# Kernel optimization log

Measured on AMD Instinct MI355X. Metric: run time of the kernel, lower is better.

Reference implementation:

```python
import jax, jax.numpy as jnp
import numpy as np

N_SLICES, H, W = 64, 64, 64
VD, VH, VW = 64, 64, 64
K = 3            # PSF kernel size per axis
RES = 1.5        # res_s / res_r
GAP = 1.0        # through-plane slice spacing in recon voxels
N_ITER = 2       # CG iterations (init kwarg)


def _rotmat(ax, ay, az):
    cx, sx = np.cos(ax), np.sin(ax)
    cy, sy = np.cos(ay), np.sin(ay)
    cz, sz = np.cos(az), np.sin(az)
    Rx = np.array([[1, 0, 0], [0, cx, -sx], [0, sx, cx]])
    Ry = np.array([[cy, 0, sy], [0, 1, 0], [-sy, 0, cy]])
    Rz = np.array([[cz, -sz, 0], [sz, cz, 0], [0, 0, 1]])
    return Rz @ Ry @ Rx


def setup_inputs() -> dict:
    rng = np.random.default_rng(0)
    R = np.stack([_rotmat(*rng.normal(0.0, 0.05, 3)) for _ in range(N_SLICES)])
    t = np.zeros((N_SLICES, 3))
    t[:, :2] = rng.normal(0.0, 1.0, (N_SLICES, 2))
    t[:, 2] = (np.arange(N_SLICES) - (N_SLICES - 1) / 2) * GAP + rng.normal(0.0, 0.3, N_SLICES)
    transforms = jnp.asarray(np.concatenate([R, t[:, :, None]], -1), jnp.float32)  # (S,3,4)
    k1, k2 = jax.random.split(jax.random.key(0))
    slices = jax.random.uniform(k1, (N_SLICES, H, W), jnp.float32)
    volume = jax.random.uniform(k2, (VD, VH, VW), jnp.float32) * 0.1
    g = np.arange(K) - (K - 1) / 2
    gz, gy, gx = np.meshgrid(g, g, g, indexing='ij')
    psf = np.exp(-(gx ** 2 + gy ** 2) / (2 * 0.6 ** 2) - gz ** 2 / (2 * 1.0 ** 2))
    psf = jnp.asarray(psf / psf.sum(), jnp.float32)
    return {"transforms": transforms, "slices": slices, "volume": volume, "psf": psf}


def _positions(transforms):
    # PSF sample positions of every slice pixel, mapped into volume voxel coords (xyz).
    xs = (jnp.arange(W) - (W - 1) / 2) * RES
    ys = (jnp.arange(H) - (H - 1) / 2) * RES
    o = jnp.arange(K) - (K - 1) / 2
    oz, oy, ox = jnp.meshgrid(o, o, o, indexing='ij')
    off = jnp.stack([ox, oy, oz], -1).reshape(-1, 3)              # (K^3, 3)
    base = jnp.stack(jnp.broadcast_arrays(xs[None, :], ys[:, None], jnp.zeros((H, W))), -1)
    pts = base[None] + off[:, None, None, :]                      # (K^3, H, W, 3) slice frame
    R, tr = transforms[:, :, :3], transforms[:, :, 3]
    pos = jnp.einsum('sij,khwj->skhwi', R, pts) + tr[:, None, None, None, :]
    center = jnp.array([(VW - 1) / 2, (VH - 1) / 2, (VD - 1) / 2], jnp.float32)
    return pos + center                                           # (S, K^3, H, W, 3)


def _corner_iter(pos):
    # yields the 8 trilinear corners: (clipped int indices (z,y,x), weight with OOB zeroed)
    x, y, z = pos[..., 0], pos[..., 1], pos[..., 2]
    x0, y0, z0 = jnp.floor(x), jnp.floor(y), jnp.floor(z)
    fx, fy, fz = x - x0, y - y0, z - z0
    for dz in (0, 1):
        for dy in (0, 1):
            for dx in (0, 1):
                xi, yi, zi = x0 + dx, y0 + dy, z0 + dz
                w = (fx if dx else 1 - fx) * (fy if dy else 1 - fy) * (fz if dz else 1 - fz)
                valid = (xi >= 0) & (xi < VW) & (yi >= 0) & (yi < VH) & (zi >= 0) & (zi < VD)
                w = jnp.where(valid, w, 0.0)
                yield (jnp.clip(zi, 0, VD - 1).astype(jnp.int32),
                       jnp.clip(yi, 0, VH - 1).astype(jnp.int32),
                       jnp.clip(xi, 0, VW - 1).astype(jnp.int32)), w


def _A(vol, pos, psf_flat):
    # slice_acquisition: trilinear gather + PSF-weighted sum -> (S,H,W)
    acc = jnp.zeros(pos.shape[:-1], vol.dtype)
    for (zi, yi, xi), w in _corner_iter(pos):
        acc = acc + w * vol[zi, yi, xi]
    return jnp.einsum('k,skhw->shw', psf_flat, acc)


def _At(slc, pos, psf_flat):
    # slice_acquisition_adjoint: PSF-weighted trilinear scatter-add -> (VD,VH,VW)
    vals = psf_flat[None, :, None, None] * slc[:, None]           # (S,K^3,H,W)
    vol = jnp.zeros((VD, VH, VW), slc.dtype)
    for (zi, yi, xi), w in _corner_iter(pos):
        vol = vol.at[zi, yi, xi].add(w * vals)
    return vol


def _cg(Afun, b, x0, n_iter):
    x = x0
    r = b - Afun(x)
    p = r
    rr = jnp.vdot(r, r)
    for i in range(n_iter):
        Ap = Afun(p)
        alpha = rr / jnp.vdot(p, Ap)
        x = x + alpha * p
        if i == n_iter - 1:
            break
        r = r - alpha * Ap
        rr_new = jnp.vdot(r, r)
        p = r + (rr_new / rr) * p
        rr = rr_new
    return x


def reference(transforms, slices, volume, psf):
    pos = _positions(transforms)
    psf_flat = psf.reshape(-1)
    AtA = lambda v: _At(_A(v, pos, psf_flat), pos, psf_flat)
    b = _At(slices, pos, psf_flat)
    x = _cg(AtA, b, volume, N_ITER)
    return jax.nn.relu(x)
```

## Files before the change

### kernel.cpp

```cpp
#include <hip/hip_runtime.h>

typedef __attribute__((ext_vector_type(2))) float f32x2;

#define NS 64
#define HH 64
#define WW 64
#define VD 64
#define VH 64
#define VW 64
#define NVOX (VD*VH*VW)
#define NPIX (NS*HH*WW)
#define RES 1.5f
#define NTAB (NS*27)
#define WIN 6
#define SPLIT 4
#define COL_PAD 67
#define GP_ROW 68
#define GP_SLC (66*GP_ROW)
#define GP_TOT (NS*GP_SLC)

__global__ __launch_bounds__(256) void k_setup(const float* __restrict__ tr,
                                               const float* __restrict__ psf,
                                               float* __restrict__ tab) {
    int i = blockIdx.x * 256 + threadIdx.x;
    if (i >= NTAB) return;
    int s = i / 27, k = i % 27;
    const float* p = tr + s * 12;
    float R00 = p[0], R01 = p[1], R02 = p[2],  t0 = p[3];
    float R10 = p[4], R11 = p[5], R12 = p[6],  t1 = p[7];
    float R20 = p[8], R21 = p[9], R22 = p[10], t2 = p[11];
    float Ux = RES * R00, Uy = RES * R10, Uz = RES * R20;
    float Vx = RES * R01, Vy = RES * R11, Vz = RES * R21;
    float ox = (float)(k % 3 - 1), oy = (float)((k / 3) % 3 - 1), oz = (float)(k / 9 - 1);
    float Cx = t0 + 31.5f + R00 * ox + R01 * oy + R02 * oz - 31.5f * (Ux + Vx);
    float Cy = t1 + 31.5f + R10 * ox + R11 * oy + R12 * oz - 31.5f * (Uy + Vy);
    float Cz = t2 + 31.5f + R20 * ox + R21 * oy + R22 * oz - 31.5f * (Uz + Vz);
    float inv = 1.f / (Ux * Vy - Uy * Vx);
    float* e = tab + i * 16;
    e[0] = Vy * inv;  e[1] = -Uy * inv;  e[2] = -Vx * inv; e[3] = Ux * inv;
    e[4] = Ux; e[5] = Uy; e[6] = Vx; e[7] = Vy;
    e[8] = Uz; e[9] = Vz; e[10] = Cx; e[11] = Cy;
    e[12] = Cz; e[13] = psf[k]; e[14] = 0.f; e[15] = 0.f;
}

__device__ __forceinline__ float trilin_gather_bf(const float* __restrict__ vol,
                                                  float px, float py, float pz) {
    float x0 = floorf(px), y0 = floorf(py), z0 = floorf(pz);
    float fx = px - x0, fy = py - y0, fz = pz - z0;
    int ix = (int)x0, iy = (int)y0, iz = (int)z0;

    float wx0 = ((unsigned)ix       < 64u) ? (1.f - fx) : 0.f;
    float wx1 = ((unsigned)(ix + 1) < 64u) ? fx         : 0.f;
    float wy0 = ((unsigned)iy       < 64u) ? (1.f - fy) : 0.f;
    float wy1 = ((unsigned)(iy + 1) < 64u) ? fy         : 0.f;
    float wz0 = ((unsigned)iz       < 64u) ? (1.f - fz) : 0.f;
    float wz1 = ((unsigned)(iz + 1) < 64u) ? fz         : 0.f;

    int xc0 = min(max(ix, 0), 63),     xc1 = min(max(ix + 1, 0), 63);
    int yc0 = min(max(iy, 0), 63) << 6,  yc1 = min(max(iy + 1, 0), 63) << 6;
    int zc0 = min(max(iz, 0), 63) << 12, zc1 = min(max(iz + 1, 0), 63) << 12;

    float v000 = vol[zc0 + yc0 + xc0], v001 = vol[zc0 + yc0 + xc1];
    float v010 = vol[zc0 + yc1 + xc0], v011 = vol[zc0 + yc1 + xc1];
    float v100 = vol[zc1 + yc0 + xc0], v101 = vol[zc1 + yc0 + xc1];
    float v110 = vol[zc1 + yc1 + xc0], v111 = vol[zc1 + yc1 + xc1];

    float w00 = wx0 * wy0, w01 = wx1 * wy0, w10 = wx0 * wy1, w11 = wx1 * wy1;
    float lo = fmaf(w00, v000, fmaf(w01, v001, fmaf(w10, v010, w11 * v011)));
    float hi = fmaf(w00, v100, fmaf(w01, v101, fmaf(w10, v110, w11 * v111)));
    return fmaf(wz0, lo, wz1 * hi);
}

template<bool SUB>
__global__ __launch_bounds__(256) void k_a(const float* __restrict__ vin,
                                           float* __restrict__ gp,
                                           const float* __restrict__ tr,
                                           const float* __restrict__ psf,
                                           const float* __restrict__ slc) {
    __shared__ float s_psf[27];
    if (threadIdx.x < 27) s_psf[threadIdx.x] = psf[threadIdx.x];
    __syncthreads();
    int gid = blockIdx.x * 256 + threadIdx.x;
    int pixel = gid >> 2, q = gid & 3;
    int s = pixel >> 12;
    int pix = pixel & 4095;
    int h = pix >> 6, w = pix & 63;
    const float* p = tr + s * 12;
    float R0 = p[0], R1 = p[1], R2 = p[2],  t0 = p[3];
    float R3 = p[4], R4 = p[5], R5 = p[6],  t1 = p[7];
    float R6 = p[8], R7 = p[9], R8 = p[10], t2 = p[11];
    float xs = ((float)w - 31.5f) * RES;
    float ys = ((float)h - 31.5f) * RES;
    float p0x = fmaf(R0, xs, fmaf(R1, ys, t0)) + 31.5f;
    float p0y = fmaf(R3, xs, fmaf(R4, ys, t1)) + 31.5f;
    float p0z = fmaf(R6, xs, fmaf(R7, ys, t2)) + 31.5f;
    float a = 0.f;
#pragma unroll
    for (int j = 0; j < 7; ++j) {
        int k = q + 4 * j;
        if (k < 27) {
            float ox = (float)(k % 3 - 1), oy = (float)((k / 3) % 3 - 1), oz = (float)(k / 9 - 1);
            float px = p0x + ox * R0 + oy * R1 + oz * R2;
            float py = p0y + ox * R3 + oy * R4 + oz * R5;
            float pz = p0z + ox * R6 + oy * R7 + oz * R8;
            a = fmaf(s_psf[k], trilin_gather_bf(vin, px, py, pz), a);
        }
    }
    a += __shfl_xor(a, 1);
    a += __shfl_xor(a, 2);
    if (q == 0) gp[s * GP_SLC + (h + 1) * GP_ROW + (w + 1)] = SUB ? (slc[pixel] - a) : a;
}

__device__ __forceinline__ void block_reduce_atomic(float v, float* dst) {
#pragma unroll
    for (int off = 32; off > 0; off >>= 1) v += __shfl_down(v, off, 64);
    __shared__ float s_red[4];
    int lane = threadIdx.x & 63, wid = threadIdx.x >> 6;
    if (lane == 0) s_red[wid] = v;
    __syncthreads();
    if (threadIdx.x == 0) atomicAdd(dst, s_red[0] + s_red[1] + s_red[2] + s_red[3]);
}

__global__ __launch_bounds__(512, 4) void k_atv(const float* __restrict__ g,
                                                float* __restrict__ part,
                                                const float* __restrict__ tab) {
    __shared__ float stab[16 * 27 * 16];
    __shared__ float cols[32][COL_PAD];

    int tid = threadIdx.x;
    int Yb    = blockIdx.x >> 3;
    int xhalf = (blockIdx.x >> 2) & 1;
    int split = blockIdx.x & 3;

    {
        const float4* src = (const float4*)(tab + split * 16 * 27 * 16);
        float4* dst = (float4*)stab;
#pragma unroll
        for (int i = 0; i < 4; ++i) {
            int j = tid + i * 512;
            if (j < 1728) dst[j] = src[j];
        }
    }
    {
        float4* c4 = (float4*)&cols[0][0];
#pragma unroll
        for (int i = 0; i < 2; ++i) {
            int j = tid + i * 512;
            if (j < 536) c4[j] = make_float4(0.f, 0.f, 0.f, 0.f);
        }
    }
    __syncthreads();

    int xl = tid & 31;
    int sg = tid >> 5;
    int s  = split * 16 + sg;
    float X = (float)(xhalf * 32 + xl);
    float Y = (float)Yb;

    const float* tb = stab + sg * 27 * 16;
    int gbase = s * GP_SLC;

    {
    }
    const float* ec = tb + 13 * 16;
    float4 ce0 = *(const float4*)(ec);
    float4 ce2 = *(const float4*)(ec + 8);
    float4 ce3 = *(const float4*)(ec + 12);
    float rxc = X - ce2.z, ryc = Y - ce2.w;
    float wsc = ce0.x * rxc + ce0.z * ryc;
    float hsc = ce0.y * rxc + ce0.w * ryc;
    float pzc = fmaf(wsc, ce2.x, fmaf(hsc, ce2.y, ce3.x));
    float basef = floorf(pzc) - 2.f;
    int   basei = (int)basef;

    f32x2 a01 = {0.f, 0.f}, a23 = {0.f, 0.f}, a45 = {0.f, 0.f};
    const f32x2 zero2 = {0.f, 0.f};
    const f32x2 cA0 = {1.f, 2.f}, cB0 = {-1.f, 0.f};
    const f32x2 cA1 = {3.f, 4.f}, cB1 = {1.f, 2.f};
    const f32x2 cA2 = {5.f, 6.f}, cB2 = {3.f, 4.f};

#pragma unroll 3
    for (int k = 0; k < 27; ++k) {
        const float* e = tb + k * 16;
        float4 e0 = *(const float4*)(e);
        float4 e1 = *(const float4*)(e + 4);
        float4 e2 = *(const float4*)(e + 8);
        float4 e3 = *(const float4*)(e + 12);
        float rx = X - e2.z, ry = Y - e2.w;
        float ws = e0.x * rx + e0.z * ry;
        float hs = e0.y * rx + e0.w * ry;
        float w0f = __builtin_amdgcn_fmed3f(floorf(ws), -1.f, 63.f);
        float h0f = __builtin_amdgcn_fmed3f(floorf(hs), -1.f, 63.f);
        int wA = (int)w0f, hA = (int)h0f;
        float Ux = e1.x, Uy = e1.y, Vx = e1.z, Vy = e1.w;
        float Uz = e2.x, Vz = e2.y;
        float Czb = e3.x - basef;
        float psfk = e3.y;
        float Cxr = -rx, Cyr = -ry;
        int colbase = gbase + wA + 1;
#pragma unroll
        for (int dh = 0; dh < 2; ++dh) {
            float fh = h0f + (float)dh;
            float tx  = fmaf(fh, Vx, Cxr);
            float ty  = fmaf(fh, Vy, Cyr);
            float tzb = fmaf(fh, Vz, Czb);
            int rowoff = colbase + (hA + 1 + dh) * GP_ROW;
#pragma unroll
            for (int dw = 0; dw < 2; ++dw) {
                float fw = w0f + (float)dw;
                float ddx = fmaf(fw, Ux, tx);
                float ddy = fmaf(fw, Uy, ty);
                float wx = fmaxf(1.f - fabsf(ddx), 0.f);
                float wy = fmaxf(1.f - fabsf(ddy), 0.f);
                float gv = g[rowoff + dw];
                float val = wx * wy * psfk * gv;
                float prel = fmaf(fw, Uz, tzb);
                f32x2 v2 = {val, val};
                f32x2 p2 = {prel, prel};
                a01 += v2 * __builtin_elementwise_max(zero2,
                          __builtin_elementwise_min(cA0 - p2, p2 - cB0));
                a23 += v2 * __builtin_elementwise_max(zero2,
                          __builtin_elementwise_min(cA1 - p2, p2 - cB1));
                a45 += v2 * __builtin_elementwise_max(zero2,
                          __builtin_elementwise_min(cA2 - p2, p2 - cB2));
            }
        }
    }

    float accs[WIN] = {a01.x, a01.y, a23.x, a23.y, a45.x, a45.y};
#pragma unroll
    for (int j = 0; j < WIN; ++j) {
        int zj = basei + j;
        int okz = ((unsigned)zj < 64u);
        int zc = min(max(zj, 0), 63);
        atomicAdd(&cols[xl][zc], okz ? accs[j] : 0.f);
    }
    __syncthreads();

    float* pout = part + split * NVOX + (Yb << 6) + xhalf * 32;
#pragma unroll
    for (int i = 0; i < 4; ++i) {
        int j = tid + i * 512;
        int z = j >> 5, x = j & 31;
        pout[(z << 12) + x] = cols[x][z];
    }
}


__device__ __forceinline__ float sum4p(const float* __restrict__ part, int i) {
    return (part[i] + part[NVOX + i]) + (part[2 * NVOX + i] + part[3 * NVOX + i]);
}

__global__ __launch_bounds__(256) void k_residual4(const float* __restrict__ part,
                                                   float* __restrict__ r,
                                                   float* __restrict__ p,
                                                   float* __restrict__ scal) {
    int i = blockIdx.x * 256 + threadIdx.x;
    float rv = sum4p(part, i);
    r[i] = rv;
    p[i] = rv;
    block_reduce_atomic(rv * rv, &scal[0]);
}

__global__ __launch_bounds__(256) void k_dot_reduce4(const float* __restrict__ part,
                                                     const float* __restrict__ p,
                                                     float* __restrict__ Ap,
                                                     float* __restrict__ dst) {
    int i = blockIdx.x * 256 + threadIdx.x;
    float apv = sum4p(part, i);
    Ap[i] = apv;
    block_reduce_atomic(p[i] * apv, dst);
}

__global__ __launch_bounds__(256) void k_dot4(const float* __restrict__ part,
                                              const float* __restrict__ p,
                                              float* __restrict__ dst) {
    int i = blockIdx.x * 256 + threadIdx.x;
    block_reduce_atomic(p[i] * sum4p(part, i), dst);
}

__global__ __launch_bounds__(256) void k_update_xr(const float* __restrict__ x_in,
                                                   float* __restrict__ x_out,
                                                   float* __restrict__ r,
                                                   const float* __restrict__ p,
                                                   const float* __restrict__ Ap,
                                                   float* __restrict__ scal) {
    int i = blockIdx.x * 256 + threadIdx.x;
    float alpha = scal[0] / scal[1];
    x_out[i] = fmaf(alpha, p[i], x_in[i]);
    float rv = fmaf(-alpha, Ap[i], r[i]);
    r[i] = rv;
    block_reduce_atomic(rv * rv, &scal[2]);
}

__global__ __launch_bounds__(256) void k_update_p(float* __restrict__ p,
                                                  const float* __restrict__ r,
                                                  const float* __restrict__ scal) {
    int i = blockIdx.x * 256 + threadIdx.x;
    float beta = scal[2] / scal[0];
    p[i] = fmaf(beta, p[i], r[i]);
}

__global__ __launch_bounds__(256) void k_final(const float* __restrict__ x,
                                               const float* __restrict__ p,
                                               const float* __restrict__ scal,
                                               float* __restrict__ out) {
    int i = blockIdx.x * 256 + threadIdx.x;
    float alpha = scal[2] / scal[3];
    float v = fmaf(alpha, p[i], x[i]);
    out[i] = v > 0.f ? v : 0.f;
}

extern "C" void kernel_launch(void* const* d_in, const int* in_sizes, int n_in,
                              void* d_out, int out_size, void* d_ws, size_t ws_size,
                              hipStream_t stream) {
    const float* transforms = (const float*)d_in[0];
    const float* slices     = (const float*)d_in[1];
    const float* volume     = (const float*)d_in[2];
    const float* psf        = (const float*)d_in[3];
    float* out = (float*)d_out;

    float* tab    = (float*)d_ws;
    float* gbuf   = tab    + NTAB * 16;
    float* scal   = gbuf   + GP_TOT;
    float* part   = scal   + 8;
    float* vol_x  = part   + SPLIT * NVOX;
    float* vol_r  = vol_x  + NVOX;
    float* vol_p  = vol_r  + NVOX;
    float* Ap     = vol_p  + NVOX;

    const int ablk = 64 * 2 * SPLIT;
    const int fblk = NPIX * 4 / 256;
    const int vblk = NVOX / 256;

    hipMemsetAsync(gbuf, 0, (GP_TOT + 8) * sizeof(float), stream);

    k_setup<<<(NTAB + 255) / 256, 256, 0, stream>>>(transforms, psf, tab);

    k_a<true><<<fblk, 256, 0, stream>>>(volume, gbuf, transforms, psf, slices);
    k_atv<<<ablk, 512, 0, stream>>>(gbuf, part, tab);
    k_residual4<<<vblk, 256, 0, stream>>>(part, vol_r, vol_p, scal);

    k_a<false><<<fblk, 256, 0, stream>>>(vol_p, gbuf, transforms, psf, nullptr);
    k_atv<<<ablk, 512, 0, stream>>>(gbuf, part, tab);
    k_dot_reduce4<<<vblk, 256, 0, stream>>>(part, vol_p, Ap, &scal[1]);
    k_update_xr<<<vblk, 256, 0, stream>>>(volume, vol_x, vol_r, vol_p, Ap, scal);
    k_update_p<<<vblk, 256, 0, stream>>>(vol_p, vol_r, scal);

    k_a<false><<<fblk, 256, 0, stream>>>(vol_p, gbuf, transforms, psf, nullptr);
    k_atv<<<ablk, 512, 0, stream>>>(gbuf, part, tab);
    k_dot4<<<vblk, 256, 0, stream>>>(part, vol_p, &scal[3]);
    k_final<<<vblk, 256, 0, stream>>>(vol_x, vol_p, scal, out);
}
```

Before: 289.9 us.

## Restructure forward and adjoint kernels: per-pixel threads, per-wave slices, eight-way split

```diff
diff --git a/kernel.cpp b/kernel.cpp
--- a/kernel.cpp
+++ b/kernel.cpp
@@ -1,6 +1,4 @@
 #include <hip/hip_runtime.h>
-
-typedef __attribute__((ext_vector_type(2))) float f32x2;
 
 #define NS 64
 #define HH 64
@@ -13,7 +11,7 @@
 #define RES 1.5f
 #define NTAB (NS*27)
 #define WIN 6
-#define SPLIT 4
+#define SPLIT 8
 #define COL_PAD 67
 #define GP_ROW 68
 #define GP_SLC (66*GP_ROW)
@@ -81,10 +79,8 @@
     if (threadIdx.x < 27) s_psf[threadIdx.x] = psf[threadIdx.x];
     __syncthreads();
     int gid = blockIdx.x * 256 + threadIdx.x;
-    int pixel = gid >> 2, q = gid & 3;
-    int s = pixel >> 12;
-    int pix = pixel & 4095;
-    int h = pix >> 6, w = pix & 63;
+    int s = gid >> 12;
+    int h = (gid >> 6) & 63, w = gid & 63;
     const float* p = tr + s * 12;
     float R0 = p[0], R1 = p[1], R2 = p[2],  t0 = p[3];
     float R3 = p[4], R4 = p[5], R5 = p[6],  t1 = p[7];
@@ -96,19 +92,17 @@
     float p0z = fmaf(R6, xs, fmaf(R7, ys, t2)) + 31.5f;
     float a = 0.f;
 #pragma unroll
-    for (int j = 0; j < 7; ++j) {
-        int k = q + 4 * j;
-        if (k < 27) {
-            float ox = (float)(k % 3 - 1), oy = (float)((k / 3) % 3 - 1), oz = (float)(k / 9 - 1);
-            float px = p0x + ox * R0 + oy * R1 + oz * R2;
-            float py = p0y + ox * R3 + oy * R4 + oz * R5;
-            float pz = p0z + ox * R6 + oy * R7 + oz * R8;
-            a = fmaf(s_psf[k], trilin_gather_bf(vin, px, py, pz), a);
-        }
-    }
-    a += __shfl_xor(a, 1);
-    a += __shfl_xor(a, 2);
-    if (q == 0) gp[s * GP_SLC + (h + 1) * GP_ROW + (w + 1)] = SUB ? (slc[pixel] - a) : a;
+    for (int k = 0; k < 27; ++k) {
+        const float ox = (float)(k % 3 - 1), oy = (float)((k / 3) % 3 - 1), oz = (float)(k / 9 - 1);
+        float px = p0x + ox * R0 + oy * R1 + oz * R2;
+        float py = p0y + ox * R3 + oy * R4 + oz * R5;
+        float pz = p0z + ox * R6 + oy * R7 + oz * R8;
+        bool inb = (px > -1.f) & (px < 64.f) & (py > -1.f) & (py < 64.f)
+                 & (pz > -1.f) & (pz < 64.f);
+        if (inb) a = fmaf(s_psf[k], trilin_gather_bf(vin, px, py, pz), a);
+    }
+    float outv = SUB ? (slc[gid] - a) : a;
+    gp[s * GP_SLC + (h + 1) * GP_ROW + (w + 1)] = outv;
 }
 
 __device__ __forceinline__ void block_reduce_atomic(float v, float* dst) {
@@ -121,47 +115,31 @@
     if (threadIdx.x == 0) atomicAdd(dst, s_red[0] + s_red[1] + s_red[2] + s_red[3]);
 }
 
-__global__ __launch_bounds__(512, 4) void k_atv(const float* __restrict__ g,
+__global__ __launch_bounds__(512, 2) void k_atv(const float* __restrict__ g,
                                                 float* __restrict__ part,
                                                 const float* __restrict__ tab) {
-    __shared__ float stab[16 * 27 * 16];
-    __shared__ float cols[32][COL_PAD];
-
+    __shared__ float cols[64][COL_PAD];
     int tid = threadIdx.x;
-    int Yb    = blockIdx.x >> 3;
-    int xhalf = (blockIdx.x >> 2) & 1;
-    int split = blockIdx.x & 3;
-
-    {
-        const float4* src = (const float4*)(tab + split * 16 * 27 * 16);
-        float4* dst = (float4*)stab;
-#pragma unroll
-        for (int i = 0; i < 4; ++i) {
-            int j = tid + i * 512;
-            if (j < 1728) dst[j] = src[j];
-        }
-    }
     {
         float4* c4 = (float4*)&cols[0][0];
 #pragma unroll
-        for (int i = 0; i < 2; ++i) {
+        for (int i = 0; i < 3; ++i) {
             int j = tid + i * 512;
-            if (j < 536) c4[j] = make_float4(0.f, 0.f, 0.f, 0.f);
+            if (j < 1072) c4[j] = make_float4(0.f, 0.f, 0.f, 0.f);
         }
     }
     __syncthreads();
 
-    int xl = tid & 31;
-    int sg = tid >> 5;
-    int s  = split * 16 + sg;
-    float X = (float)(xhalf * 32 + xl);
-    float Y = (float)Yb;
-
-    const float* tb = stab + sg * 27 * 16;
+    int Yb    = blockIdx.x >> 3;
+    int split = blockIdx.x & 7;
+    int lane  = tid & 63;
+    int wave  = tid >> 6;
+    int s = __builtin_amdgcn_readfirstlane(split * 8 + wave);
+    float X = (float)lane, Y = (float)Yb;
+
+    const float* tb = tab + s * 27 * 16;
     int gbase = s * GP_SLC;
 
-    {
-    }
     const float* ec = tb + 13 * 16;
     float4 ce0 = *(const float4*)(ec);
     float4 ce2 = *(const float4*)(ec + 8);
@@ -173,11 +151,9 @@
     float basef = floorf(pzc) - 2.f;
     int   basei = (int)basef;
 
-    f32x2 a01 = {0.f, 0.f}, a23 = {0.f, 0.f}, a45 = {0.f, 0.f};
-    const f32x2 zero2 = {0.f, 0.f};
-    const f32x2 cA0 = {1.f, 2.f}, cB0 = {-1.f, 0.f};
-    const f32x2 cA1 = {3.f, 4.f}, cB1 = {1.f, 2.f};
-    const f32x2 cA2 = {5.f, 6.f}, cB2 = {3.f, 4.f};
+    float acc[WIN];
+#pragma unroll
+    for (int j = 0; j < WIN; ++j) acc[j] = 0.f;
 
 #pragma unroll 3
     for (int k = 0; k < 27; ++k) {
@@ -215,68 +191,67 @@
                 float gv = g[rowoff + dw];
                 float val = wx * wy * psfk * gv;
                 float prel = fmaf(fw, Uz, tzb);
-                f32x2 v2 = {val, val};
-                f32x2 p2 = {prel, prel};
-                a01 += v2 * __builtin_elementwise_max(zero2,
-                          __builtin_elementwise_min(cA0 - p2, p2 - cB0));
-                a23 += v2 * __builtin_elementwise_max(zero2,
-                          __builtin_elementwise_min(cA1 - p2, p2 - cB1));
-                a45 += v2 * __builtin_elementwise_max(zero2,
-                          __builtin_elementwise_min(cA2 - p2, p2 - cB2));
+#pragma unroll
+                for (int j = 0; j < WIN; ++j) {
+                    float t = fmaxf(0.f, 1.f - fabsf(prel - (float)j));
+                    acc[j] = fmaf(val, t, acc[j]);
+                }
             }
         }
     }
 
-    float accs[WIN] = {a01.x, a01.y, a23.x, a23.y, a45.x, a45.y};
 #pragma unroll
     for (int j = 0; j < WIN; ++j) {
         int zj = basei + j;
         int okz = ((unsigned)zj < 64u);
         int zc = min(max(zj, 0), 63);
-        atomicAdd(&cols[xl][zc], okz ? accs[j] : 0.f);
+        atomicAdd(&cols[lane][zc], okz ? acc[j] : 0.f);
     }
     __syncthreads();
 
-    float* pout = part + split * NVOX + (Yb << 6) + xhalf * 32;
-#pragma unroll
-    for (int i = 0; i < 4; ++i) {
+    float* pout = part + split * NVOX + (Yb << 6);
+#pragma unroll
+    for (int i = 0; i < 8; ++i) {
         int j = tid + i * 512;
-        int z = j >> 5, x = j & 31;
+        int z = j >> 6, x = j & 63;
         pout[(z << 12) + x] = cols[x][z];
     }
 }
 
 
-__device__ __forceinline__ float sum4p(const float* __restrict__ part, int i) {
-    return (part[i] + part[NVOX + i]) + (part[2 * NVOX + i] + part[3 * NVOX + i]);
-}
-
-__global__ __launch_bounds__(256) void k_residual4(const float* __restrict__ part,
+__device__ __forceinline__ float sum8(const float* __restrict__ part, int i) {
+    float a = 0.f;
+#pragma unroll
+    for (int j = 0; j < SPLIT; ++j) a += part[j * NVOX + i];
+    return a;
+}
+
+__global__ __launch_bounds__(256) void k_residual8(const float* __restrict__ part,
                                                    float* __restrict__ r,
                                                    float* __restrict__ p,
                                                    float* __restrict__ scal) {
     int i = blockIdx.x * 256 + threadIdx.x;
-    float rv = sum4p(part, i);
+    float rv = sum8(part, i);
     r[i] = rv;
     p[i] = rv;
     block_reduce_atomic(rv * rv, &scal[0]);
 }
 
-__global__ __launch_bounds__(256) void k_dot_reduce4(const float* __restrict__ part,
+__global__ __launch_bounds__(256) void k_dot_reduce8(const float* __restrict__ part,
                                                      const float* __restrict__ p,
                                                      float* __restrict__ Ap,
                                                      float* __restrict__ dst) {
     int i = blockIdx.x * 256 + threadIdx.x;
-    float apv = sum4p(part, i);
+    float apv = sum8(part, i);
     Ap[i] = apv;
     block_reduce_atomic(p[i] * apv, dst);
 }
 
-__global__ __launch_bounds__(256) void k_dot4(const float* __restrict__ part,
+__global__ __launch_bounds__(256) void k_dot8(const float* __restrict__ part,
                                               const float* __restrict__ p,
                                               float* __restrict__ dst) {
     int i = blockIdx.x * 256 + threadIdx.x;
-    block_reduce_atomic(p[i] * sum4p(part, i), dst);
+    block_reduce_atomic(p[i] * sum8(part, i), dst);
 }
 
 __global__ __launch_bounds__(256) void k_update_xr(const float* __restrict__ x_in,
@@ -329,8 +304,8 @@
     float* vol_p  = vol_r  + NVOX;
     float* Ap     = vol_p  + NVOX;
 
-    const int ablk = 64 * 2 * SPLIT;
-    const int fblk = NPIX * 4 / 256;
+    const int ablk = 64 * SPLIT;
+    const int fblk = NPIX / 256;
     const int vblk = NVOX / 256;
 
     hipMemsetAsync(gbuf, 0, (GP_TOT + 8) * sizeof(float), stream);
@@ -339,16 +314,16 @@
 
     k_a<true><<<fblk, 256, 0, stream>>>(volume, gbuf, transforms, psf, slices);
     k_atv<<<ablk, 512, 0, stream>>>(gbuf, part, tab);
-    k_residual4<<<vblk, 256, 0, stream>>>(part, vol_r, vol_p, scal);
+    k_residual8<<<vblk, 256, 0, stream>>>(part, vol_r, vol_p, scal);
 
     k_a<false><<<fblk, 256, 0, stream>>>(vol_p, gbuf, transforms, psf, nullptr);
     k_atv<<<ablk, 512, 0, stream>>>(gbuf, part, tab);
-    k_dot_reduce4<<<vblk, 256, 0, stream>>>(part, vol_p, Ap, &scal[1]);
+    k_dot_reduce8<<<vblk, 256, 0, stream>>>(part, vol_p, Ap, &scal[1]);
     k_update_xr<<<vblk, 256, 0, stream>>>(volume, vol_x, vol_r, vol_p, Ap, scal);
     k_update_p<<<vblk, 256, 0, stream>>>(vol_p, vol_r, scal);
 
     k_a<false><<<fblk, 256, 0, stream>>>(vol_p, gbuf, transforms, psf, nullptr);
     k_atv<<<ablk, 512, 0, stream>>>(gbuf, part, tab);
-    k_dot4<<<vblk, 256, 0, stream>>>(part, vol_p, &scal[3]);
+    k_dot8<<<vblk, 256, 0, stream>>>(part, vol_p, &scal[3]);
     k_final<<<vblk, 256, 0, stream>>>(vol_x, vol_p, scal, out);
 }
```

Measured after the change: 273.1 us. -5.8%, faster.
